# Optimization experiments

Hardware: AMD Instinct MI355X
Metric: run time of the kernel (lower is better)

## Reference

```python
import jax, jax.numpy as jnp
import numpy as np

NX, NY = 8192, 8192
C1, C2, D = 2048, 2048, 512

def setup_inputs() -> dict:
    key = jax.random.key(0)
    k1, k2, k3, k4, k5 = jax.random.split(key, 5)
    scale1 = 1.0 / np.sqrt(C1)
    scale2 = 1.0 / np.sqrt(C2)
    return {
        "x": jax.random.normal(k1, (NX, C1), dtype=jnp.float32),
        "y": jax.random.normal(k2, (NY, C2), dtype=jnp.float32),
        "Wq": jax.random.uniform(k3, (D, C1), dtype=jnp.float32, minval=-scale1, maxval=scale1),
        "Wk": jax.random.uniform(k4, (D, C2), dtype=jnp.float32, minval=-scale2, maxval=scale2),
        "Wv": jax.random.uniform(k5, (D, C2), dtype=jnp.float32, minval=-scale2, maxval=scale2),
    }

def reference(x, y, Wq, Wk, Wv):
    d = Wq.shape[0]
    q = x @ Wq.T                      # [nx, d]
    k = y @ Wk.T                      # [ny, d]
    v = y @ Wv.T                      # [ny, d]
    a = (q @ k.T) * (d ** -0.5)       # [nx, ny]
    # torch.triu(ones) masks upper triangle INCLUDING diagonal -> zero where j >= i
    nx, ny = a.shape
    i = jnp.arange(nx)[:, None]
    j = jnp.arange(ny)[None, :]
    a = jnp.where(j >= i, 0.0, a)
    return a @ v                      # [nx, d]
```

## Files before the change

### kernel.cpp

```cpp
#include <hip/hip_runtime.h>
#include <hip/hip_bf16.h>


typedef __bf16 bf16x8 __attribute__((ext_vector_type(8)));
typedef __bf16 bf16x4 __attribute__((ext_vector_type(4)));
typedef float f32x4 __attribute__((ext_vector_type(4)));

#define MFMA16(a, b, c) __builtin_amdgcn_mfma_f32_16x16x32_bf16(a, b, c, 0, 0, 0)

constexpr float SCALE = 0.04419417382415922f;

__device__ __forceinline__ void ld16(const void* g, void* l) {
    __builtin_amdgcn_global_load_lds(
        (__attribute__((address_space(1))) void*)g,
        (__attribute__((address_space(3))) void*)l, 16, 0, 0);
}

__device__ __forceinline__ bf16x8 frag(const __bf16* base, int r, int c) {
    return *(const bf16x8*)((const char*)base + r * 128 + ((c ^ (r & 7)) * 16));
}

__device__ __forceinline__ bf16x8 fragA32(const float* base, int r, int c0) {
    const char* rowp = (const char*)base + r * 256;
    f32x4 a = *(const f32x4*)(rowp + ((c0 ^ (r & 15)) * 16));
    f32x4 b = *(const f32x4*)(rowp + (((c0 + 1) ^ (r & 15)) * 16));
    bf16x8 o;
    o[0] = (__bf16)a[0]; o[1] = (__bf16)a[1];
    o[2] = (__bf16)a[2]; o[3] = (__bf16)a[3];
    o[4] = (__bf16)b[0]; o[5] = (__bf16)b[1];
    o[6] = (__bf16)b[2]; o[7] = (__bf16)b[3];
    return o;
}

__device__ inline bf16x4 pack4(float4 a) {
    bf16x4 r;
    r[0] = (__bf16)a.x; r[1] = (__bf16)a.y;
    r[2] = (__bf16)a.z; r[3] = (__bf16)a.w;
    return r;
}

__global__ __launch_bounds__(256) void convert_w(
    const float* __restrict__ wqf, const float* __restrict__ wkf,
    const float* __restrict__ wvf, __bf16* __restrict__ wqb,
    __bf16* __restrict__ wkb, __bf16* __restrict__ wvb)
{
    const size_t tid = (size_t)blockIdx.x * 256 + threadIdx.x;
    const size_t w = tid >> 6;
    const int lane = (int)(tid & 63);
    size_t f = w * 512;
    const float* src; __bf16* dst;
    if (f < 1048576)      { src = wqf; dst = wqb; }
    else if (f < 2097152) { src = wkf; dst = wkb; f -= 1048576; }
    else                  { src = wvf; dst = wvb; f -= 2097152; }
    const float4* s4 = (const float4*)(src + f);
    float4 a = s4[lane];
    float4 b = s4[64 + lane];
    __bf16* d = dst + f;
    *(bf16x4*)(d + lane * 4)       = pack4(a);
    *(bf16x4*)(d + 256 + lane * 4) = pack4(b);
}

__global__ __launch_bounds__(256, 2) void gemm_qkv2(
    const float* __restrict__ x, const float* __restrict__ y,
    const __bf16* __restrict__ wq, const __bf16* __restrict__ wk,
    const __bf16* __restrict__ wv, __bf16* __restrict__ qo,
    __bf16* __restrict__ ko, __bf16* __restrict__ kT,
    __bf16* __restrict__ vT)
{
    constexpr int K = 2048, N = 512;
    __shared__ __align__(16) float  Asf[128][64];
    __shared__ __align__(16) __bf16 Bs[2][128][64];

    const bool iskv = (blockIdx.y & 1) != 0;
    const float* A = iskv ? y : x;
    const __bf16* B0 = iskv ? wk : wq;

    const int tid  = threadIdx.x;
    const int wave = tid >> 6, lane = tid & 63;
    const int fr = lane & 15, fq = lane >> 4;
    const int m0 = blockIdx.x * 128, n0 = (blockIdx.y >> 1) * 128;
    const int wr = (wave >> 1) * 64, wc = (wave & 1) * 64;
    const int lr = lane >> 3;
    const int cd = (lane & 7) ^ lr;
    const int lr4 = lane >> 4;
    const int cl  = lane & 15;

    f32x4 acc0[4][4], acc1[4][4];
#pragma unroll
    for (int a = 0; a < 4; ++a)
#pragma unroll
        for (int b = 0; b < 4; ++b) {
            acc0[a][b] = f32x4{0.f, 0.f, 0.f, 0.f};
            acc1[a][b] = f32x4{0.f, 0.f, 0.f, 0.f};
        }

    const __bf16* bg0 = B0 + (size_t)(n0 + wave * 32 + lr) * K + cd * 8;
    const __bf16* bg1 = wv + (size_t)(n0 + wave * 32 + lr) * K + cd * 8;
    float*  alf = &Asf[wave * 32][0];
    __bf16* bl0 = &Bs[0][wave * 32][0];
    __bf16* bl1 = &Bs[1][wave * 32][0];
    const float* ag0 = A + (size_t)(m0 + wave * 32 + lr4) * K;

    for (int kk = 0; kk < K; kk += 64) {
        __syncthreads();
#pragma unroll
        for (int u = 0; u < 4; ++u)
            ld16(bg0 + (size_t)(u * 8) * K + kk, bl0 + u * 512);
        if (iskv) {
#pragma unroll
            for (int u = 0; u < 4; ++u)
                ld16(bg1 + (size_t)(u * 8) * K + kk, bl1 + u * 512);
        }
#pragma unroll
        for (int u = 0; u < 8; ++u) {
            const int rw = u * 4 + lr4;
            const int c  = cl ^ (rw & 15);
            ld16(ag0 + (size_t)(u * 4) * K + kk + c * 4, alf + u * 256);
        }
        __syncthreads();
#pragma unroll
        for (int ks = 0; ks < 2; ++ks) {
            bf16x8 af[4], bf[4];
#pragma unroll
            for (int rt = 0; rt < 4; ++rt)
                af[rt] = fragA32(&Asf[0][0], wr + rt * 16 + fr, ks * 8 + fq * 2);
#pragma unroll
            for (int nt = 0; nt < 4; ++nt)
                bf[nt] = frag(&Bs[0][0][0], wc + nt * 16 + fr, ks * 4 + fq);
#pragma unroll
            for (int rt = 0; rt < 4; ++rt)
#pragma unroll
                for (int nt = 0; nt < 4; ++nt)
                    acc0[rt][nt] = MFMA16(af[rt], bf[nt], acc0[rt][nt]);
            if (iskv) {
                bf16x8 bg[4];
#pragma unroll
                for (int nt = 0; nt < 4; ++nt)
                    bg[nt] = frag(&Bs[1][0][0], wc + nt * 16 + fr, ks * 4 + fq);
#pragma unroll
                for (int rt = 0; rt < 4; ++rt)
#pragma unroll
                    for (int nt = 0; nt < 4; ++nt)
                        acc1[rt][nt] = MFMA16(af[rt], bg[nt], acc1[rt][nt]);
            }
        }
    }

    if (!iskv) {
#pragma unroll
        for (int rt = 0; rt < 4; ++rt)
#pragma unroll
            for (int nt = 0; nt < 4; ++nt) {
                const int col = n0 + wc + nt * 16 + fr;
#pragma unroll
                for (int r = 0; r < 4; ++r) {
                    const int row = m0 + wr + rt * 16 + fq * 4 + r;
                    qo[(size_t)row * N + col] = (__bf16)(acc0[rt][nt][r] * SCALE);
                }
            }
    } else {
#pragma unroll
        for (int rt = 0; rt < 4; ++rt)
#pragma unroll
            for (int nt = 0; nt < 4; ++nt) {
                const int col  = n0 + wc + nt * 16 + fr;
                const int row0 = m0 + wr + rt * 16 + fq * 4;
                bf16x4 k4, v4;
#pragma unroll
                for (int r = 0; r < 4; ++r) {
                    k4[r] = (__bf16)acc0[rt][nt][r];
                    v4[r] = (__bf16)acc1[rt][nt][r];
                    ko[(size_t)(row0 + r) * N + col] = k4[r];
                }
                *(bf16x4*)(kT + (size_t)col * 8192 + row0) = k4;
                *(bf16x4*)(vT + (size_t)col * 8192 + row0) = v4;
            }
    }
}

__global__ __launch_bounds__(256, 3) void hs_gemm(
    const __bf16* __restrict__ vT, const __bf16* __restrict__ kT,
    const __bf16* __restrict__ q, const __bf16* __restrict__ k,
    __bf16* __restrict__ Ht, __bf16* __restrict__ Sd)
{
    __shared__ __align__(16) __bf16 As[128][64];
    __shared__ __align__(16) __bf16 Bs[128][64];

    const int tid  = threadIdx.x;
    const int wave = tid >> 6, lane = tid & 63;
    const int fr = lane & 15, fq = lane >> 4;
    const int wr = (wave >> 1) * 64, wc = (wave & 1) * 64;
    const int lr = lane >> 3;
    const int cd = (lane & 7) ^ lr;

    f32x4 acc[4][4];
#pragma unroll
    for (int a = 0; a < 4; ++a)
#pragma unroll
        for (int b = 0; b < 4; ++b) acc[a][b] = f32x4{0.f, 0.f, 0.f, 0.f};

    __bf16* al = &As[wave * 32][0];
    __bf16* bl = &Bs[wave * 32][0];

    if (blockIdx.y < 63) {
        const int c  = blockIdx.y;
        const int m0 = (blockIdx.x & 3) * 128;
        const int n0 = (blockIdx.x >> 2) * 128;

        const __bf16* ag = vT + (size_t)(m0 + wave * 32 + lr) * 8192 + c * 128 + cd * 8;
        const __bf16* bg = kT + (size_t)(n0 + wave * 32 + lr) * 8192 + c * 128 + cd * 8;

        for (int kk = 0; kk < 128; kk += 64) {
            __syncthreads();
#pragma unroll
            for (int u = 0; u < 4; ++u) {
                ld16(ag + (size_t)(u * 8) * 8192 + kk, al + u * 512);
                ld16(bg + (size_t)(u * 8) * 8192 + kk, bl + u * 512);
            }
            __syncthreads();
#pragma unroll
            for (int ks = 0; ks < 2; ++ks) {
                bf16x8 af[4], bf[4];
#pragma unroll
                for (int rt = 0; rt < 4; ++rt)
                    af[rt] = frag(&As[0][0], wr + rt * 16 + fr, ks * 4 + fq);
#pragma unroll
                for (int nt = 0; nt < 4; ++nt)
                    bf[nt] = frag(&Bs[0][0], wc + nt * 16 + fr, ks * 4 + fq);
#pragma unroll
                for (int rt = 0; rt < 4; ++rt)
#pragma unroll
                    for (int nt = 0; nt < 4; ++nt)
                        acc[rt][nt] = MFMA16(af[rt], bf[nt], acc[rt][nt]);
            }
        }

        __bf16* tp = Ht + (size_t)c * 262144;
#pragma unroll
        for (int rt = 0; rt < 4; ++rt)
#pragma unroll
            for (int nt = 0; nt < 4; ++nt) {
                const int col = n0 + wc + nt * 16 + fr;
#pragma unroll
                for (int r = 0; r < 4; ++r) {
                    const int row = m0 + wr + rt * 16 + fq * 4 + r;
                    tp[(size_t)row * 512 + col] = (__bf16)acc[rt][nt][r];
                }
            }
    } else {
        const int t = (blockIdx.y - 63) * 16 + blockIdx.x;

        const __bf16* ag = q + (size_t)(t * 128 + wave * 32 + lr) * 512 + cd * 8;
        const __bf16* bg = k + (size_t)(t * 128 + wave * 32 + lr) * 512 + cd * 8;

        for (int kk = 0; kk < 512; kk += 64) {
            __syncthreads();
#pragma unroll
            for (int u = 0; u < 4; ++u) {
                ld16(ag + (size_t)(u * 8) * 512 + kk, al + u * 512);
                ld16(bg + (size_t)(u * 8) * 512 + kk, bl + u * 512);
            }
            __syncthreads();
#pragma unroll
            for (int ks = 0; ks < 2; ++ks) {
                bf16x8 af[4], bf[4];
#pragma unroll
                for (int rt = 0; rt < 4; ++rt)
                    af[rt] = frag(&As[0][0], wr + rt * 16 + fr, ks * 4 + fq);
#pragma unroll
                for (int nt = 0; nt < 4; ++nt)
                    bf[nt] = frag(&Bs[0][0], wc + nt * 16 + fr, ks * 4 + fq);
#pragma unroll
                for (int rt = 0; rt < 4; ++rt)
#pragma unroll
                    for (int nt = 0; nt < 4; ++nt)
                        acc[rt][nt] = MFMA16(af[rt], bf[nt], acc[rt][nt]);
            }
        }

        __bf16* tp = Sd + (size_t)t * 16384;
#pragma unroll
        for (int rt = 0; rt < 4; ++rt)
#pragma unroll
            for (int nt = 0; nt < 4; ++nt) {
                const int col = wc + nt * 16 + fr;
#pragma unroll
                for (int r = 0; r < 4; ++r) {
                    const int row = wr + rt * 16 + fq * 4 + r;
                    float vv = (col < row) ? acc[rt][nt][r] : 0.f;
                    tp[row * 128 + col] = (__bf16)vv;
                }
            }
    }
}

__global__ __launch_bounds__(256) void prefix_scan(
    const __bf16* __restrict__ Ht, __bf16* __restrict__ Pt)
{
    const size_t e = ((size_t)blockIdx.x * 256 + threadIdx.x) * 4;
    float a0 = 0.f, a1 = 0.f, a2 = 0.f, a3 = 0.f;
#pragma unroll 7
    for (int c = 0; c < 63; ++c) {
        bf16x4 h = *(const bf16x4*)(Ht + (size_t)c * 262144 + e);
        a0 += (float)h[0]; a1 += (float)h[1];
        a2 += (float)h[2]; a3 += (float)h[3];
        bf16x4 p;
        p[0] = (__bf16)a0; p[1] = (__bf16)a1;
        p[2] = (__bf16)a2; p[3] = (__bf16)a3;
        *(bf16x4*)(Pt + (size_t)(c + 1) * 262144 + e) = p;
    }
}

__global__ __launch_bounds__(256, 3) void out_gemm(
    const __bf16* __restrict__ q, const __bf16* __restrict__ Sd,
    const __bf16* __restrict__ vT, const __bf16* __restrict__ Pt,
    float* __restrict__ out)
{
    __shared__ __align__(16) __bf16 As[128][64];
    __shared__ __align__(16) __bf16 Bs[128][64];

    const int t  = blockIdx.x;
    const int n0 = blockIdx.y * 128;

    const int tid  = threadIdx.x;
    const int wave = tid >> 6, lane = tid & 63;
    const int fr = lane & 15, fq = lane >> 4;
    const int wr = (wave >> 1) * 64, wc = (wave & 1) * 64;
    const int lr = lane >> 3;
    const int cd = (lane & 7) ^ lr;
    const int srow = wave * 32 + lr;

    f32x4 acc[4][4];
#pragma unroll
    for (int a = 0; a < 4; ++a)
#pragma unroll
        for (int b = 0; b < 4; ++b) acc[a][b] = f32x4{0.f, 0.f, 0.f, 0.f};

    __bf16* al = &As[wave * 32][0];
    __bf16* bl = &Bs[wave * 32][0];

    if (t > 0) {
        const __bf16* ag = q + (size_t)(t * 128 + srow) * 512 + cd * 8;
        const __bf16* bg2 = Pt + (size_t)t * 262144
                          + (size_t)(n0 + srow) * 512 + cd * 8;
        for (int kk = 0; kk < 512; kk += 64) {
            __syncthreads();
#pragma unroll
            for (int u = 0; u < 4; ++u) {
                ld16(ag + (size_t)(u * 8) * 512 + kk, al + u * 512);
                ld16(bg2 + (size_t)(u * 8) * 512 + kk, bl + u * 512);
            }
            __syncthreads();
#pragma unroll
            for (int ks = 0; ks < 2; ++ks) {
                bf16x8 af[4], bf[4];
#pragma unroll
                for (int rt = 0; rt < 4; ++rt)
                    af[rt] = frag(&As[0][0], wr + rt * 16 + fr, ks * 4 + fq);
#pragma unroll
                for (int nt = 0; nt < 4; ++nt)
                    bf[nt] = frag(&Bs[0][0], wc + nt * 16 + fr, ks * 4 + fq);
#pragma unroll
                for (int rt = 0; rt < 4; ++rt)
#pragma unroll
                    for (int nt = 0; nt < 4; ++nt)
                        acc[rt][nt] = MFMA16(af[rt], bf[nt], acc[rt][nt]);
            }
        }
    }

    const __bf16* at3 = Sd + (size_t)t * 16384 + (size_t)srow * 128 + cd * 8;
    const __bf16* bg3 = vT + (size_t)(n0 + srow) * 8192 + t * 128 + cd * 8;
    for (int kk = 0; kk < 128; kk += 64) {
        __syncthreads();
#pragma unroll
        for (int u = 0; u < 4; ++u) {
            ld16(at3 + (size_t)(u * 8) * 128 + kk, al + u * 512);
            ld16(bg3 + (size_t)(u * 8) * 8192 + kk, bl + u * 512);
        }
        __syncthreads();
#pragma unroll
        for (int ks = 0; ks < 2; ++ks) {
            bf16x8 af[4], bf[4];
#pragma unroll
            for (int rt = 0; rt < 4; ++rt)
                af[rt] = frag(&As[0][0], wr + rt * 16 + fr, ks * 4 + fq);
#pragma unroll
            for (int nt = 0; nt < 4; ++nt)
                bf[nt] = frag(&Bs[0][0], wc + nt * 16 + fr, ks * 4 + fq);
#pragma unroll
            for (int rt = 0; rt < 4; ++rt)
#pragma unroll
                for (int nt = 0; nt < 4; ++nt)
                    acc[rt][nt] = MFMA16(af[rt], bf[nt], acc[rt][nt]);
        }
    }

#pragma unroll
    for (int rt = 0; rt < 4; ++rt)
#pragma unroll
        for (int nt = 0; nt < 4; ++nt) {
            const int col = n0 + wc + nt * 16 + fr;
#pragma unroll
            for (int r = 0; r < 4; ++r) {
                const int row = t * 128 + wr + rt * 16 + fq * 4 + r;
                out[(size_t)row * 512 + col] = acc[rt][nt][r];
            }
        }
}

extern "C" void kernel_launch(void* const* d_in, const int* in_sizes, int n_in,
                              void* d_out, int out_size, void* d_ws, size_t ws_size,
                              hipStream_t stream) {
    const float* x  = (const float*)d_in[0];
    const float* y  = (const float*)d_in[1];
    const float* Wq = (const float*)d_in[2];
    const float* Wk = (const float*)d_in[3];
    const float* Wv = (const float*)d_in[4];
    float* out = (float*)d_out;

    const size_t QK = (size_t)8192 * 512;
    __bf16* q  = (__bf16*)d_ws;
    __bf16* k  = q + QK;
    __bf16* kT = k + QK;
    __bf16* vT = kT + QK;
    __bf16* Ht  = vT + QK;
    __bf16* Pt  = Ht + 16777216;
    __bf16* wqb = Pt + 16777216;
    __bf16* wkb = wqb + 1048576;
    __bf16* wvb = wkb + 1048576;
    __bf16* Sd = wqb;

    convert_w<<<1536, 256, 0, stream>>>(Wq, Wk, Wv, wqb, wkb, wvb);
    gemm_qkv2<<<dim3(64, 8), 256, 0, stream>>>(x, y, wqb, wkb, wvb, q, k, kT, vT);
    hs_gemm<<<dim3(16, 67), 256, 0, stream>>>(vT, kT, q, k, Ht, Sd);
    prefix_scan<<<256, 256, 0, stream>>>(Ht, Pt);
    out_gemm<<<dim3(64, 4), 256, 0, stream>>>(q, Sd, vT, Pt, out);
}
```

Before: 254.7 us.

## Double-buffer LDS staging in QKV projection and output GEMMs

The QKV projection GEMM now stages 32-wide K slices into two LDS buffers, prefetching the next slice while MFMAs run on the current one. It uses a new swizzle layout for the fp32 A and bf16 B tiles. The output GEMM merges its prefix-state and diagonal-block loops into one double-buffered staged loop with a single barrier per step. The goal is to hide global-to-LDS load latency behind compute. The cost is more LDS per block, so out_gemm's occupancy hint drops from 3 to 2 blocks per CU.

```diff
diff --git a/kernel.cpp b/kernel.cpp
--- a/kernel.cpp
+++ b/kernel.cpp
@@ -20,16 +20,21 @@
     return *(const bf16x8*)((const char*)base + r * 128 + ((c ^ (r & 7)) * 16));
 }
 
-__device__ __forceinline__ bf16x8 fragA32(const float* base, int r, int c0) {
-    const char* rowp = (const char*)base + r * 256;
-    f32x4 a = *(const f32x4*)(rowp + ((c0 ^ (r & 15)) * 16));
-    f32x4 b = *(const f32x4*)(rowp + (((c0 + 1) ^ (r & 15)) * 16));
+__device__ __forceinline__ bf16x8 fragA32(const float* base, int r, int fq) {
+    const char* rowp = (const char*)base + r * 128;
+    const int c0 = fq * 2;
+    f32x4 a = *(const f32x4*)(rowp + ((c0 ^ (r & 7)) * 16));
+    f32x4 b = *(const f32x4*)(rowp + (((c0 + 1) ^ (r & 7)) * 16));
     bf16x8 o;
     o[0] = (__bf16)a[0]; o[1] = (__bf16)a[1];
     o[2] = (__bf16)a[2]; o[3] = (__bf16)a[3];
     o[4] = (__bf16)b[0]; o[5] = (__bf16)b[1];
     o[6] = (__bf16)b[2]; o[7] = (__bf16)b[3];
     return o;
+}
+
+__device__ __forceinline__ bf16x8 fragB32(const __bf16* base, int r, int fq) {
+    return *(const bf16x8*)((const char*)base + r * 64 + ((fq ^ (r & 3)) * 16));
 }
 
 __device__ inline bf16x4 pack4(float4 a) {
@@ -68,8 +73,8 @@
     __bf16* __restrict__ vT)
 {
     constexpr int K = 2048, N = 512;
-    __shared__ __align__(16) float  Asf[128][64];
-    __shared__ __align__(16) __bf16 Bs[2][128][64];
+    __shared__ __align__(16) float  Asf[2][128][32];
+    __shared__ __align__(16) __bf16 Bs[2][2][128][32];
 
     const bool iskv = (blockIdx.y & 1) != 0;
     const float* A = iskv ? y : x;
@@ -80,10 +85,10 @@
     const int fr = lane & 15, fq = lane >> 4;
     const int m0 = blockIdx.x * 128, n0 = (blockIdx.y >> 1) * 128;
     const int wr = (wave >> 1) * 64, wc = (wave & 1) * 64;
-    const int lr = lane >> 3;
-    const int cd = (lane & 7) ^ lr;
-    const int lr4 = lane >> 4;
-    const int cl  = lane & 15;
+    const int lr  = lane >> 3;
+    const int cd  = (lane & 7) ^ lr;
+    const int lr2 = lane >> 2;
+    const int cb  = (lane & 3) ^ (lr2 & 3);
 
     f32x4 acc0[4][4], acc1[4][4];
 #pragma unroll
@@ -94,56 +99,58 @@
             acc1[a][b] = f32x4{0.f, 0.f, 0.f, 0.f};
         }
 
-    const __bf16* bg0 = B0 + (size_t)(n0 + wave * 32 + lr) * K + cd * 8;
-    const __bf16* bg1 = wv + (size_t)(n0 + wave * 32 + lr) * K + cd * 8;
-    float*  alf = &Asf[wave * 32][0];
-    __bf16* bl0 = &Bs[0][wave * 32][0];
-    __bf16* bl1 = &Bs[1][wave * 32][0];
-    const float* ag0 = A + (size_t)(m0 + wave * 32 + lr4) * K;
-
-    for (int kk = 0; kk < K; kk += 64) {
+    const float*  ag  = A  + (size_t)(m0 + wave * 32 + lr) * K + cd * 4;
+    const __bf16* bg0 = B0 + (size_t)(n0 + wave * 32 + lr2) * K + cb * 8;
+    const __bf16* bg1 = wv + (size_t)(n0 + wave * 32 + lr2) * K + cb * 8;
+
+    auto stg = [&](int kks, int buf) {
+        float* al = &Asf[buf][wave * 32][0];
+#pragma unroll
+        for (int u = 0; u < 4; ++u)
+            ld16(ag + (size_t)(u * 8) * K + kks, al + u * 256);
+        __bf16* b0 = &Bs[buf][0][wave * 32][0];
+#pragma unroll
+        for (int u = 0; u < 2; ++u)
+            ld16(bg0 + (size_t)(u * 16) * K + kks, b0 + u * 512);
+        if (iskv) {
+            __bf16* b1 = &Bs[buf][1][wave * 32][0];
+#pragma unroll
+            for (int u = 0; u < 2; ++u)
+                ld16(bg1 + (size_t)(u * 16) * K + kks, b1 + u * 512);
+        }
+    };
+
+    stg(0, 0);
+    __syncthreads();
+
+    for (int s = 0; s < 64; ++s) {
+        const int buf = s & 1;
+        if (s < 63) stg((s + 1) * 32, buf ^ 1);
+
+        bf16x8 af[4], bf[4];
+#pragma unroll
+        for (int rt = 0; rt < 4; ++rt)
+            af[rt] = fragA32(&Asf[buf][0][0], wr + rt * 16 + fr, fq);
+#pragma unroll
+        for (int nt = 0; nt < 4; ++nt)
+            bf[nt] = fragB32(&Bs[buf][0][0][0], wc + nt * 16 + fr, fq);
+#pragma unroll
+        for (int rt = 0; rt < 4; ++rt)
+#pragma unroll
+            for (int nt = 0; nt < 4; ++nt)
+                acc0[rt][nt] = MFMA16(af[rt], bf[nt], acc0[rt][nt]);
+        if (iskv) {
+            bf16x8 bv[4];
+#pragma unroll
+            for (int nt = 0; nt < 4; ++nt)
+                bv[nt] = fragB32(&Bs[buf][1][0][0], wc + nt * 16 + fr, fq);
+#pragma unroll
+            for (int rt = 0; rt < 4; ++rt)
+#pragma unroll
+                for (int nt = 0; nt < 4; ++nt)
+                    acc1[rt][nt] = MFMA16(af[rt], bv[nt], acc1[rt][nt]);
+        }
         __syncthreads();
-#pragma unroll
-        for (int u = 0; u < 4; ++u)
-            ld16(bg0 + (size_t)(u * 8) * K + kk, bl0 + u * 512);
-        if (iskv) {
-#pragma unroll
-            for (int u = 0; u < 4; ++u)
-                ld16(bg1 + (size_t)(u * 8) * K + kk, bl1 + u * 512);
-        }
-#pragma unroll
-        for (int u = 0; u < 8; ++u) {
-            const int rw = u * 4 + lr4;
-            const int c  = cl ^ (rw & 15);
-            ld16(ag0 + (size_t)(u * 4) * K + kk + c * 4, alf + u * 256);
-        }
-        __syncthreads();
-#pragma unroll
-        for (int ks = 0; ks < 2; ++ks) {
-            bf16x8 af[4], bf[4];
-#pragma unroll
-            for (int rt = 0; rt < 4; ++rt)
-                af[rt] = fragA32(&Asf[0][0], wr + rt * 16 + fr, ks * 8 + fq * 2);
-#pragma unroll
-            for (int nt = 0; nt < 4; ++nt)
-                bf[nt] = frag(&Bs[0][0][0], wc + nt * 16 + fr, ks * 4 + fq);
-#pragma unroll
-            for (int rt = 0; rt < 4; ++rt)
-#pragma unroll
-                for (int nt = 0; nt < 4; ++nt)
-                    acc0[rt][nt] = MFMA16(af[rt], bf[nt], acc0[rt][nt]);
-            if (iskv) {
-                bf16x8 bg[4];
-#pragma unroll
-                for (int nt = 0; nt < 4; ++nt)
-                    bg[nt] = frag(&Bs[1][0][0], wc + nt * 16 + fr, ks * 4 + fq);
-#pragma unroll
-                for (int rt = 0; rt < 4; ++rt)
-#pragma unroll
-                    for (int nt = 0; nt < 4; ++nt)
-                        acc1[rt][nt] = MFMA16(af[rt], bg[nt], acc1[rt][nt]);
-            }
-        }
     }
 
     if (!iskv) {
@@ -311,13 +318,13 @@
     }
 }
 
-__global__ __launch_bounds__(256, 3) void out_gemm(
+__global__ __launch_bounds__(256, 2) void out_gemm(
     const __bf16* __restrict__ q, const __bf16* __restrict__ Sd,
     const __bf16* __restrict__ vT, const __bf16* __restrict__ Pt,
     float* __restrict__ out)
 {
-    __shared__ __align__(16) __bf16 As[128][64];
-    __shared__ __align__(16) __bf16 Bs[128][64];
+    __shared__ __align__(16) __bf16 As[2][128][64];
+    __shared__ __align__(16) __bf16 Bs[2][128][64];
 
     const int t  = blockIdx.x;
     const int n0 = blockIdx.y * 128;
@@ -336,64 +343,49 @@
 #pragma unroll
         for (int b = 0; b < 4; ++b) acc[a][b] = f32x4{0.f, 0.f, 0.f, 0.f};
 
-    __bf16* al = &As[wave * 32][0];
-    __bf16* bl = &Bs[wave * 32][0];
-
-    if (t > 0) {
-        const __bf16* ag = q + (size_t)(t * 128 + srow) * 512 + cd * 8;
-        const __bf16* bg2 = Pt + (size_t)t * 262144
-                          + (size_t)(n0 + srow) * 512 + cd * 8;
-        for (int kk = 0; kk < 512; kk += 64) {
-            __syncthreads();
-#pragma unroll
-            for (int u = 0; u < 4; ++u) {
-                ld16(ag + (size_t)(u * 8) * 512 + kk, al + u * 512);
-                ld16(bg2 + (size_t)(u * 8) * 512 + kk, bl + u * 512);
-            }
-            __syncthreads();
-#pragma unroll
-            for (int ks = 0; ks < 2; ++ks) {
-                bf16x8 af[4], bf[4];
-#pragma unroll
-                for (int rt = 0; rt < 4; ++rt)
-                    af[rt] = frag(&As[0][0], wr + rt * 16 + fr, ks * 4 + fq);
-#pragma unroll
-                for (int nt = 0; nt < 4; ++nt)
-                    bf[nt] = frag(&Bs[0][0], wc + nt * 16 + fr, ks * 4 + fq);
-#pragma unroll
-                for (int rt = 0; rt < 4; ++rt)
-#pragma unroll
-                    for (int nt = 0; nt < 4; ++nt)
-                        acc[rt][nt] = MFMA16(af[rt], bf[nt], acc[rt][nt]);
-            }
-        }
-    }
-
-    const __bf16* at3 = Sd + (size_t)t * 16384 + (size_t)srow * 128 + cd * 8;
-    const __bf16* bg3 = vT + (size_t)(n0 + srow) * 8192 + t * 128 + cd * 8;
-    for (int kk = 0; kk < 128; kk += 64) {
-        __syncthreads();
+    const __bf16* qB  = q  + (size_t)(t * 128 + srow) * 512 + cd * 8;
+    const __bf16* ptB = Pt + (size_t)t * 262144 + (size_t)(n0 + srow) * 512 + cd * 8;
+    const __bf16* sdB = Sd + (size_t)t * 16384 + (size_t)srow * 128 + cd * 8;
+    const __bf16* vtB = vT + (size_t)(n0 + srow) * 8192 + t * 128 + cd * 8;
+
+    const int ns = (t > 0) ? 10 : 2;
+
+    auto stg = [&](int s, int buf) {
+        const __bf16 *ap, *bp; size_t sa, sb;
+        if (t > 0 && s < 8) { ap = qB + s * 64;  sa = 512;  bp = ptB + s * 64; sb = 512; }
+        else { const int sc = (t > 0) ? s - 8 : s;
+               ap = sdB + sc * 64; sa = 128; bp = vtB + sc * 64; sb = 8192; }
+        __bf16* al = &As[buf][wave * 32][0];
+        __bf16* bl = &Bs[buf][wave * 32][0];
 #pragma unroll
         for (int u = 0; u < 4; ++u) {
-            ld16(at3 + (size_t)(u * 8) * 128 + kk, al + u * 512);
-            ld16(bg3 + (size_t)(u * 8) * 8192 + kk, bl + u * 512);
-        }
-        __syncthreads();
+            ld16(ap + (size_t)(u * 8) * sa, al + u * 512);
+            ld16(bp + (size_t)(u * 8) * sb, bl + u * 512);
+        }
+    };
+
+    stg(0, 0);
+    __syncthreads();
+
+    for (int s = 0; s < ns; ++s) {
+        const int buf = s & 1;
+        if (s + 1 < ns) stg(s + 1, buf ^ 1);
 #pragma unroll
         for (int ks = 0; ks < 2; ++ks) {
             bf16x8 af[4], bf[4];
 #pragma unroll
             for (int rt = 0; rt < 4; ++rt)
-                af[rt] = frag(&As[0][0], wr + rt * 16 + fr, ks * 4 + fq);
+                af[rt] = frag(&As[buf][0][0], wr + rt * 16 + fr, ks * 4 + fq);
 #pragma unroll
             for (int nt = 0; nt < 4; ++nt)
-                bf[nt] = frag(&Bs[0][0], wc + nt * 16 + fr, ks * 4 + fq);
+                bf[nt] = frag(&Bs[buf][0][0], wc + nt * 16 + fr, ks * 4 + fq);
 #pragma unroll
             for (int rt = 0; rt < 4; ++rt)
 #pragma unroll
                 for (int nt = 0; nt < 4; ++nt)
                     acc[rt][nt] = MFMA16(af[rt], bf[nt], acc[rt][nt]);
         }
+        __syncthreads();
     }
 
 #pragma unroll
```

New measurement: 275.4 us. +8.1%, slower.
